# Optimization experiments

Hardware: AMD Instinct MI355X
Metric: run time of the kernel (lower is better)

## Reference

```python
import jax, jax.numpy as jnp
import numpy as np

N, T = 4, 2048
FEAT, VEC = 512, 16          # feat_size, vec_size
K = 8192                     # codebook_size = prediction_encoder.output_size
CIN = 512                    # prediction_encoder.input_size
OFFSET = 0
IGNORE = -100                # torch CrossEntropyLoss default ignore_index
EPS = 1e-12                  # torch F.normalize eps


def setup_inputs() -> dict:
    key = jax.random.key(0)
    k1, k2, k3, k4, k5, k6 = jax.random.split(key, 6)
    feats = jax.random.normal(k1, (N, T, FEAT), dtype=jnp.float32)
    context = jax.random.normal(k2, (N, T, CIN), dtype=jnp.float32)
    lens = jax.random.randint(k3, (N,), T // 2, T + 1, dtype=jnp.int32)
    # xavier_normal_ for (feat_size, vec_size)
    proj_matrix = jax.random.normal(k4, (FEAT, VEC), dtype=jnp.float32) * np.sqrt(2.0 / (FEAT + VEC))
    cb = jax.random.normal(k5, (K, VEC), dtype=jnp.float32)
    codebook = cb / jnp.maximum(jnp.linalg.norm(cb, axis=1, keepdims=True), EPS)
    W_enc = jax.random.normal(k6, (CIN, K), dtype=jnp.float32) / np.sqrt(CIN)
    b_enc = jnp.zeros((K,), dtype=jnp.float32)
    return {"feats": feats, "context": context, "lens": lens,
            "proj_matrix": proj_matrix, "codebook": codebook,
            "W_enc": W_enc, "b_enc": b_enc}


def reference(feats, context, lens, proj_matrix, codebook, W_enc, b_enc):
    # prediction encoder: Linear(CIN -> K), lens unchanged
    logits = jnp.einsum("ntc,ck->ntk", context, W_enc) + b_enc      # (N,T,K)

    # --- target computation (no_grad in torch) ---
    f = feats[:, OFFSET:] @ proj_matrix                              # (N,T',V)
    f = f / jnp.maximum(jnp.linalg.norm(f, axis=-1, keepdims=True), EPS)
    # squared distance ||f - c||^2 = |f|^2 - 2 f.c + |c|^2; argmin equals
    # argmin of vector_norm since sqrt is monotone. Avoids (N,T,K,V) tensor.
    d2 = (jnp.sum(f * f, axis=-1, keepdims=True)
          - 2.0 * jnp.einsum("ntv,kv->ntk", f, codebook)
          + jnp.sum(codebook * codebook, axis=-1))                   # (N,T',K)
    targets = jnp.argmin(d2, axis=2).astype(jnp.int32)               # (N,T')
    Tp = T - OFFSET
    mask = (lens[:, None] - OFFSET) > jnp.arange(Tp)[None, :]        # (N,T')
    targets = jnp.where(mask, targets, IGNORE)

    # --- masked cross entropy (mean over non-ignored) ---
    logits_f = logits[:, OFFSET:].reshape(-1, K)                     # (N*T',K)
    targets_f = targets.reshape(-1)
    logp = jax.nn.log_softmax(logits_f, axis=-1)
    valid = targets_f != IGNORE
    safe_t = jnp.where(valid, targets_f, 0)
    nll = -jnp.take_along_axis(logp, safe_t[:, None], axis=1)[:, 0]
    loss = jnp.sum(nll * valid) / jnp.maximum(jnp.sum(valid), 1)
    return loss
```

## Files before the change

### kernel.cpp

```cpp
#include <hip/hip_runtime.h>
#include <hip/hip_bf16.h>
#include <hip/hip_fp8.h>

#define MROWS 8192
#define KDIM  512
#define NCOL  8192
#define TSEQ  2048

typedef float f32x4 __attribute__((ext_vector_type(4)));

__device__ __forceinline__ unsigned int pack4_fp8(float a, float b, float c, float d) {
#if __has_builtin(__builtin_amdgcn_cvt_pk_fp8_f32)
  int r = __builtin_amdgcn_cvt_pk_fp8_f32(a, b, 0, false);
  r = __builtin_amdgcn_cvt_pk_fp8_f32(c, d, r, true);
  return (unsigned int)r;
#else
  __hip_fp8_e4m3 ha(a), hb(b), hc(c), hd(d);
  return (unsigned int)ha.__x | ((unsigned int)hb.__x << 8) |
         ((unsigned int)hc.__x << 16) | ((unsigned int)hd.__x << 24);
#endif
}

__device__ __forceinline__ float fp8d(unsigned char b) {
  unsigned int s = b >> 7, e = (b >> 3) & 15, m = b & 7;
  if (e == 0) {
    float v = (float)m * 0.001953125f;
    return s ? -v : v;
  }
  unsigned int bits = (s << 31) | ((e + 120) << 23) | (m << 20);
  return __uint_as_float(bits);
}

__global__ void prep_kernel(const float* __restrict__ X, unsigned char* __restrict__ A8,
                            const float* __restrict__ W, unsigned char* __restrict__ B8,
                            const float* __restrict__ feats, const float* __restrict__ proj,
                            float* __restrict__ F, unsigned long long* __restrict__ amin,
                            float* __restrict__ rowsum, float* __restrict__ out) {
  __shared__ float tile[64][65];
  const int tid = threadIdx.x;
  int b = blockIdx.x;
  if (b < 4096) {
    int i = b * 256 + tid;
    float4 v = reinterpret_cast<const float4*>(X)[i];
    reinterpret_cast<unsigned int*>(A8)[i] = pack4_fp8(v.x, v.y, v.z, v.w);
  } else if (b < 5120) {
    b -= 4096;
    const int bx = b & 127, by = b >> 7;
    const int c4 = tid & 15, rr = tid >> 4;
    #pragma unroll
    for (int p = 0; p < 4; ++p) {
      int row = p * 16 + rr;
      float4 v = reinterpret_cast<const float4*>(W + (size_t)(by * 64 + row) * NCOL + bx * 64)[c4];
      tile[row][c4 * 4 + 0] = v.x; tile[row][c4 * 4 + 1] = v.y;
      tile[row][c4 * 4 + 2] = v.z; tile[row][c4 * 4 + 3] = v.w;
    }
    __syncthreads();
    #pragma unroll
    for (int p = 0; p < 4; ++p) {
      int oc = p * 16 + rr;
      unsigned int pk = pack4_fp8(tile[c4 * 4 + 0][oc], tile[c4 * 4 + 1][oc],
                                  tile[c4 * 4 + 2][oc], tile[c4 * 4 + 3][oc]);
      *reinterpret_cast<unsigned int*>(B8 + (size_t)(bx * 64 + oc) * KDIM + by * 64 + c4 * 4) = pk;
    }
  } else if (b < 5632) {
    b -= 5120;
    int rl = tid >> 4, d = tid & 15;
    int row = b * 16 + rl;
    const float4* fr4 = reinterpret_cast<const float4*>(feats + (size_t)row * KDIM);
    float acc = 0.f;
    #pragma unroll 4
    for (int kc = 0; kc < KDIM / 4; ++kc) {
      float4 v = fr4[kc];
      const float* p = proj + (size_t)kc * 64 + d;
      acc += v.x * p[0] + v.y * p[16] + v.z * p[32] + v.w * p[48];
    }
    F[(size_t)row * 16 + d] = acc;
  } else {
    int r = (b - 5632) * 256 + tid;
    amin[r] = ~0ull;
    rowsum[r] = 0.f;
    if (b == 5632 && tid == 0) out[0] = 0.f;
  }
}

#define TGT_BLOCKS 512
#define CB_CODES 128

__device__ __forceinline__ void gld16(const void* g, void* l3) {
  __builtin_amdgcn_global_load_lds((const __attribute__((address_space(1))) void*)g,
                                   (__attribute__((address_space(3))) void*)l3, 16, 0, 0);
}

__global__ __launch_bounds__(256, 4)
void gemm_targets_kernel(const unsigned char* __restrict__ A,
                         const unsigned char* __restrict__ B,
                         const float* __restrict__ bias,
                         float* __restrict__ rowsum,
                         const float* __restrict__ F,
                         const float* __restrict__ cb,
                         unsigned long long* __restrict__ amin) {
  __shared__ __align__(16) unsigned char smem[32768];
  const int tid = threadIdx.x;
  const int bid = blockIdx.x;

  if (bid < TGT_BLOCKS) {
    float (*csh)[16] = (float (*)[16])smem;
    const int r0 = (bid & 7) * 1024 + tid;
    const int c0 = (bid >> 3) * CB_CODES;
    {
      int ci = tid >> 1, half = tid & 1;
      const float4* src = reinterpret_cast<const float4*>(cb + (size_t)(c0 + ci) * 16 + half * 8);
      float4 v0 = src[0], v1 = src[1];
      float4* dst = reinterpret_cast<float4*>(&csh[ci][half * 8]);
      dst[0] = v0; dst[1] = v1;
    }
    float4 fa[4][4];
    #pragma unroll
    for (int q = 0; q < 4; ++q) {
      const float4* fp = reinterpret_cast<const float4*>(F + (size_t)(r0 + q * 256) * 16);
      fa[q][0] = fp[0]; fa[q][1] = fp[1]; fa[q][2] = fp[2]; fa[q][3] = fp[3];
    }
    __syncthreads();

    float best[4] = {3.4e38f, 3.4e38f, 3.4e38f, 3.4e38f};
    int bidx[4] = {0, 0, 0, 0};
    #pragma unroll 2
    for (int ci = 0; ci < CB_CODES; ++ci) {
      const float4* cvp = reinterpret_cast<const float4*>(&csh[ci][0]);
      float4 c0v = cvp[0], c1v = cvp[1], c2v = cvp[2], c3v = cvp[3];
      #pragma unroll
      for (int q = 0; q < 4; ++q) {
        float dot = fa[q][0].x*c0v.x + fa[q][0].y*c0v.y + fa[q][0].z*c0v.z + fa[q][0].w*c0v.w
                  + fa[q][1].x*c1v.x + fa[q][1].y*c1v.y + fa[q][1].z*c1v.z + fa[q][1].w*c1v.w
                  + fa[q][2].x*c2v.x + fa[q][2].y*c2v.y + fa[q][2].z*c2v.z + fa[q][2].w*c2v.w
                  + fa[q][3].x*c3v.x + fa[q][3].y*c3v.y + fa[q][3].z*c3v.z + fa[q][3].w*c3v.w;
        float d = -dot;
        if (d < best[q]) { best[q] = d; bidx[q] = c0 + ci; }
      }
    }
    #pragma unroll
    for (int q = 0; q < 4; ++q) {
      unsigned int u = __float_as_uint(best[q]);
      unsigned int key = (u & 0x80000000u) ? ~u : (u | 0x80000000u);
      unsigned long long pk = ((unsigned long long)key << 32) | (unsigned int)bidx[q];
      atomicMin(&amin[r0 + q * 256], pk);
    }
    return;
  }

  const int gid = bid - TGT_BLOCKS;
  const int wave = tid >> 6;
  const int lane = tid & 63;
  const int xcd = gid & 7, idx = gid >> 3;
  const int bx = xcd * 8 + (idx & 7);
  const int by = idx >> 3;
  const int row0 = by * 128;
  const int col0 = bx * 128;
  const int wr = wave >> 1, wc = wave & 1;
  unsigned char* As = smem;
  unsigned char* Bs = smem + 16384;

  f32x4 acc[4][4];
  #pragma unroll
  for (int i = 0; i < 4; ++i)
    #pragma unroll
    for (int j = 0; j < 4; ++j) acc[i][j] = (f32x4){0.f, 0.f, 0.f, 0.f};

  const int lr = lane >> 2;
  const int lcs = (((lane & 3) ^ ((lane >> 3) & 3)) << 4);

  const int l15 = lane & 15, l16 = lane >> 4;
  const int sw = (l15 >> 1) & 3;
  const int subo = (l16 & 1) * 8;
  const int lg16 = l16 >> 1;

  #pragma unroll
  for (int c = 0; c < 2; ++c) {
    int rchunk = (wave * 2 + c) * 16;
    gld16(A + (size_t)(row0 + rchunk + lr) * KDIM + lcs, As + rchunk * 64);
    gld16(B + (size_t)(col0 + rchunk + lr) * KDIM + lcs, Bs + rchunk * 64);
  }
  __syncthreads();

  #pragma unroll
  for (int t = 0; t < 8; ++t) {
    const int cur = (t & 1) * 8192;
    if (t < 7) {
      const int kt = (t + 1) * 64;
      const int nxt = ((t + 1) & 1) * 8192;
      #pragma unroll
      for (int c = 0; c < 2; ++c) {
        int rchunk = (wave * 2 + c) * 16;
        gld16(A + (size_t)(row0 + rchunk + lr) * KDIM + kt + lcs, As + nxt + rchunk * 64);
        gld16(B + (size_t)(col0 + rchunk + lr) * KDIM + kt + lcs, Bs + nxt + rchunk * 64);
      }
    }
    #pragma unroll
    for (int ks = 0; ks < 2; ++ks) {
      const int poff = (((ks * 2 + lg16) ^ sw) << 4) + subo;
      long af[4], bb[4];
      #pragma unroll
      for (int mi = 0; mi < 4; ++mi)
        af[mi] = *(const long*)(As + cur + (wr * 64 + mi * 16 + l15) * 64 + poff);
      #pragma unroll
      for (int ni = 0; ni < 4; ++ni)
        bb[ni] = *(const long*)(Bs + cur + (wc * 64 + ni * 16 + l15) * 64 + poff);
      #pragma unroll
      for (int mi = 0; mi < 4; ++mi)
        #pragma unroll
        for (int ni = 0; ni < 4; ++ni)
          acc[mi][ni] = __builtin_amdgcn_mfma_f32_16x16x32_fp8_fp8(af[mi], bb[ni], acc[mi][ni], 0, 0, 0);
    }
    if (t < 7) __syncthreads();
  }

  float bv[4];
  #pragma unroll
  for (int ni = 0; ni < 4; ++ni)
    bv[ni] = bias[col0 + wc * 64 + ni * 16 + l15];
  #pragma unroll
  for (int mi = 0; mi < 4; ++mi) {
    int rbase = row0 + wr * 64 + mi * 16 + l16 * 4;
    #pragma unroll
    for (int j = 0; j < 4; ++j) {
      float se = 0.f;
      #pragma unroll
      for (int ni = 0; ni < 4; ++ni)
        se += __expf(acc[mi][ni][j] + bv[ni]);
      #pragma unroll
      for (int o = 1; o < 16; o <<= 1) se += __shfl_xor(se, o);
      if (l15 == 0) atomicAdd(&rowsum[rbase + j], se);
    }
  }
}

__global__ void tgtloss_kernel(const unsigned char* __restrict__ A,
                               const unsigned char* __restrict__ B,
                               const float* __restrict__ bias,
                               const unsigned long long* __restrict__ amin,
                               const float* __restrict__ rowsum,
                               const int* __restrict__ lens,
                               float* __restrict__ out) {
  __shared__ float sp[4];
  const int wave = threadIdx.x >> 6, lane = threadIdx.x & 63;
  const int cnt = lens[0] + lens[1] + lens[2] + lens[3];
  const float inv = 1.0f / (float)max(cnt, 1);
  const int r = blockIdx.x * 4 + wave;
  const int tg = (int)(amin[r] & 0xffffffffull);
  uint2 ua = reinterpret_cast<const uint2*>(A + (size_t)r * KDIM)[lane];
  uint2 ub = reinterpret_cast<const uint2*>(B + (size_t)tg * KDIM)[lane];
  float s = 0.f;
  const unsigned char* pa = reinterpret_cast<const unsigned char*>(&ua);
  const unsigned char* pb = reinterpret_cast<const unsigned char*>(&ub);
  #pragma unroll
  for (int k = 0; k < 8; ++k) s += fp8d(pa[k]) * fp8d(pb[k]);
  #pragma unroll
  for (int o = 1; o < 64; o <<= 1) s += __shfl_xor(s, o);
  if (lane == 0) {
    const int n = r >> 11, t = r & (TSEQ - 1);
    sp[wave] = (t < lens[n]) ? (logf(rowsum[r]) - (s + bias[tg])) * inv : 0.f;
  }
  __syncthreads();
  if (threadIdx.x == 0)
    atomicAdd(out, sp[0] + sp[1] + sp[2] + sp[3]);
}

extern "C" void kernel_launch(void* const* d_in, const int* in_sizes, int n_in,
                              void* d_out, int out_size, void* d_ws, size_t ws_size,
                              hipStream_t stream) {
  const float* feats    = (const float*)d_in[0];
  const float* context  = (const float*)d_in[1];
  const int*   lens     = (const int*)d_in[2];
  const float* proj     = (const float*)d_in[3];
  const float* codebook = (const float*)d_in[4];
  const float* W_enc    = (const float*)d_in[5];
  const float* b_enc    = (const float*)d_in[6];
  float* out = (float*)d_out;

  char* ws = (char*)d_ws;
  unsigned char* A8 = (unsigned char*)(ws);
  unsigned char* B8 = (unsigned char*)(ws + 4194304);
  float* F          = (float*)(ws + 8388608);
  unsigned long long* amin = (unsigned long long*)(ws + 8912896);
  float* rowsum     = (float*)(ws + 8978432);

  prep_kernel<<<5664, 256, 0, stream>>>(context, A8, W_enc, B8, feats, proj, F, amin, rowsum, out);
  gemm_targets_kernel<<<TGT_BLOCKS + 4096, 256, 0, stream>>>(A8, B8, b_enc, rowsum, F, codebook, amin);
  tgtloss_kernel<<<2048, 256, 0, stream>>>(A8, B8, b_enc, amin, rowsum, lens, out);
}
```

Measured before the change: 188.5 us.

## Pre-pack FP8 operands into MFMA fragment layout and load directly from global

The prep kernel now writes the FP8 A and B matrices in a tiled layout that matches the MFMA 16x16x32 fragment order. The GEMM loads each lane's fragments straight from global memory as 16-byte vectors, with no LDS staging or barriers. The loss kernel's lookups are updated to the new layout. This removes LDS traffic and synchronisation, but each wave now reads its own operands from global/L2 with no sharing between waves through shared memory, and there is no explicit prefetch.

```diff
diff --git a/kernel.cpp b/kernel.cpp
--- a/kernel.cpp
+++ b/kernel.cpp
@@ -8,6 +8,7 @@
 #define TSEQ  2048
 
 typedef float f32x4 __attribute__((ext_vector_type(4)));
+typedef long  lx2  __attribute__((ext_vector_type(2)));
 
 __device__ __forceinline__ unsigned int pack4_fp8(float a, float b, float c, float d) {
 #if __has_builtin(__builtin_amdgcn_cvt_pk_fp8_f32)
@@ -31,6 +32,13 @@
   return __uint_as_float(bits);
 }
 
+__device__ __forceinline__ size_t pk_addr(int r, int kb) {
+  int t = kb >> 6, tb = kb & 63;
+  int ks = tb >> 5, rem = tb & 31;
+  int l16 = rem >> 3, bo = rem & 7;
+  return ((size_t)(((r >> 4) << 3) + t) << 10) + (((l16 << 4) + (r & 15)) << 4) + (ks << 3) + bo;
+}
+
 __global__ void prep_kernel(const float* __restrict__ X, unsigned char* __restrict__ A8,
                             const float* __restrict__ W, unsigned char* __restrict__ B8,
                             const float* __restrict__ feats, const float* __restrict__ proj,
@@ -41,8 +49,11 @@
   int b = blockIdx.x;
   if (b < 4096) {
     int i = b * 256 + tid;
+    int r = i >> 7;
+    int kb = (i & 127) << 2;
     float4 v = reinterpret_cast<const float4*>(X)[i];
-    reinterpret_cast<unsigned int*>(A8)[i] = pack4_fp8(v.x, v.y, v.z, v.w);
+    unsigned int pk = pack4_fp8(v.x, v.y, v.z, v.w);
+    *reinterpret_cast<unsigned int*>(A8 + pk_addr(r, kb)) = pk;
   } else if (b < 5120) {
     b -= 4096;
     const int bx = b & 127, by = b >> 7;
@@ -60,7 +71,7 @@
       int oc = p * 16 + rr;
       unsigned int pk = pack4_fp8(tile[c4 * 4 + 0][oc], tile[c4 * 4 + 1][oc],
                                   tile[c4 * 4 + 2][oc], tile[c4 * 4 + 3][oc]);
-      *reinterpret_cast<unsigned int*>(B8 + (size_t)(bx * 64 + oc) * KDIM + by * 64 + c4 * 4) = pk;
+      *reinterpret_cast<unsigned int*>(B8 + pk_addr(bx * 64 + oc, by * 64 + c4 * 4)) = pk;
     }
   } else if (b < 5632) {
     b -= 5120;
@@ -86,12 +97,7 @@
 #define TGT_BLOCKS 512
 #define CB_CODES 128
 
-__device__ __forceinline__ void gld16(const void* g, void* l3) {
-  __builtin_amdgcn_global_load_lds((const __attribute__((address_space(1))) void*)g,
-                                   (__attribute__((address_space(3))) void*)l3, 16, 0, 0);
-}
-
-__global__ __launch_bounds__(256, 4)
+__global__ __launch_bounds__(256, 3)
 void gemm_targets_kernel(const unsigned char* __restrict__ A,
                          const unsigned char* __restrict__ B,
                          const float* __restrict__ bias,
@@ -99,12 +105,11 @@
                          const float* __restrict__ F,
                          const float* __restrict__ cb,
                          unsigned long long* __restrict__ amin) {
-  __shared__ __align__(16) unsigned char smem[32768];
+  __shared__ __align__(16) float csh[CB_CODES][16];
   const int tid = threadIdx.x;
   const int bid = blockIdx.x;
 
   if (bid < TGT_BLOCKS) {
-    float (*csh)[16] = (float (*)[16])smem;
     const int r0 = (bid & 7) * 1024 + tid;
     const int c0 = (bid >> 3) * CB_CODES;
     {
@@ -157,8 +162,6 @@
   const int row0 = by * 128;
   const int col0 = bx * 128;
   const int wr = wave >> 1, wc = wave & 1;
-  unsigned char* As = smem;
-  unsigned char* Bs = smem + 16384;
 
   f32x4 acc[4][4];
   #pragma unroll
@@ -166,54 +169,34 @@
     #pragma unroll
     for (int j = 0; j < 4; ++j) acc[i][j] = (f32x4){0.f, 0.f, 0.f, 0.f};
 
-  const int lr = lane >> 2;
-  const int lcs = (((lane & 3) ^ ((lane >> 3) & 3)) << 4);
+  const unsigned char* abase[4];
+  const unsigned char* bbase[4];
+  #pragma unroll
+  for (int mi = 0; mi < 4; ++mi)
+    abase[mi] = A + ((size_t)((row0 >> 4) + wr * 4 + mi) << 13) + lane * 16;
+  #pragma unroll
+  for (int ni = 0; ni < 4; ++ni)
+    bbase[ni] = B + ((size_t)((col0 >> 4) + wc * 4 + ni) << 13) + lane * 16;
+
+  #pragma unroll
+  for (int t = 0; t < 8; ++t) {
+    lx2 afr[4], bfr[4];
+    #pragma unroll
+    for (int mi = 0; mi < 4; ++mi)
+      afr[mi] = *reinterpret_cast<const lx2*>(abase[mi] + t * 1024);
+    #pragma unroll
+    for (int ni = 0; ni < 4; ++ni)
+      bfr[ni] = *reinterpret_cast<const lx2*>(bbase[ni] + t * 1024);
+    #pragma unroll
+    for (int mi = 0; mi < 4; ++mi)
+      #pragma unroll
+      for (int ni = 0; ni < 4; ++ni) {
+        acc[mi][ni] = __builtin_amdgcn_mfma_f32_16x16x32_fp8_fp8(afr[mi][0], bfr[ni][0], acc[mi][ni], 0, 0, 0);
+        acc[mi][ni] = __builtin_amdgcn_mfma_f32_16x16x32_fp8_fp8(afr[mi][1], bfr[ni][1], acc[mi][ni], 0, 0, 0);
+      }
+  }
 
   const int l15 = lane & 15, l16 = lane >> 4;
-  const int sw = (l15 >> 1) & 3;
-  const int subo = (l16 & 1) * 8;
-  const int lg16 = l16 >> 1;
-
-  #pragma unroll
-  for (int c = 0; c < 2; ++c) {
-    int rchunk = (wave * 2 + c) * 16;
-    gld16(A + (size_t)(row0 + rchunk + lr) * KDIM + lcs, As + rchunk * 64);
-    gld16(B + (size_t)(col0 + rchunk + lr) * KDIM + lcs, Bs + rchunk * 64);
-  }
-  __syncthreads();
-
-  #pragma unroll
-  for (int t = 0; t < 8; ++t) {
-    const int cur = (t & 1) * 8192;
-    if (t < 7) {
-      const int kt = (t + 1) * 64;
-      const int nxt = ((t + 1) & 1) * 8192;
-      #pragma unroll
-      for (int c = 0; c < 2; ++c) {
-        int rchunk = (wave * 2 + c) * 16;
-        gld16(A + (size_t)(row0 + rchunk + lr) * KDIM + kt + lcs, As + nxt + rchunk * 64);
-        gld16(B + (size_t)(col0 + rchunk + lr) * KDIM + kt + lcs, Bs + nxt + rchunk * 64);
-      }
-    }
-    #pragma unroll
-    for (int ks = 0; ks < 2; ++ks) {
-      const int poff = (((ks * 2 + lg16) ^ sw) << 4) + subo;
-      long af[4], bb[4];
-      #pragma unroll
-      for (int mi = 0; mi < 4; ++mi)
-        af[mi] = *(const long*)(As + cur + (wr * 64 + mi * 16 + l15) * 64 + poff);
-      #pragma unroll
-      for (int ni = 0; ni < 4; ++ni)
-        bb[ni] = *(const long*)(Bs + cur + (wc * 64 + ni * 16 + l15) * 64 + poff);
-      #pragma unroll
-      for (int mi = 0; mi < 4; ++mi)
-        #pragma unroll
-        for (int ni = 0; ni < 4; ++ni)
-          acc[mi][ni] = __builtin_amdgcn_mfma_f32_16x16x32_fp8_fp8(af[mi], bb[ni], acc[mi][ni], 0, 0, 0);
-    }
-    if (t < 7) __syncthreads();
-  }
-
   float bv[4];
   #pragma unroll
   for (int ni = 0; ni < 4; ++ni)
@@ -247,8 +230,9 @@
   const float inv = 1.0f / (float)max(cnt, 1);
   const int r = blockIdx.x * 4 + wave;
   const int tg = (int)(amin[r] & 0xffffffffull);
-  uint2 ua = reinterpret_cast<const uint2*>(A + (size_t)r * KDIM)[lane];
-  uint2 ub = reinterpret_cast<const uint2*>(B + (size_t)tg * KDIM)[lane];
+  const int kb = lane << 3;
+  uint2 ua = *reinterpret_cast<const uint2*>(A + pk_addr(r, kb));
+  uint2 ub = *reinterpret_cast<const uint2*>(B + pk_addr(tg, kb));
   float s = 0.f;
   const unsigned char* pa = reinterpret_cast<const unsigned char*>(&ua);
   const unsigned char* pb = reinterpret_cast<const unsigned char*>(&ub);
```

Result: faster. 180.2 us (-4.4%).
